# Kernel tuning notes

Hardware: AMD Instinct MI355X
Metric: run time of the kernel (lower is better)

## Reference

```python
import jax, jax.numpy as jnp
import numpy as np

K_PRE = 500        # pre-NMS candidates per class (static-shape stand-in for boolean filter)
MAX_DET = 300      # max_detections_per_images
SCORE_THR = 0.05
NMS_THR = 0.5
MIN_SIZE = 0.01    # remove_small_boxes
BBOX_CLAMP = float(np.log(1000.0 / 16.0))


def setup_inputs():
    key = jax.random.key(0)
    k1, k2, k3, k4, k5, k6 = jax.random.split(key, 6)
    B, A, C = 2, 120000, 80
    H, W = 600, 960
    deltas = jax.random.normal(k1, (B, A, 4), jnp.float32) * 0.5
    scores = jax.random.uniform(k2, (B, A, C), jnp.float32)        # post-sigmoid class scores
    # realistic anchors: centers inside the image, sizes in [16, 256]
    cx = jax.random.uniform(k3, (B, A), jnp.float32) * W
    cy = jax.random.uniform(k4, (B, A), jnp.float32) * H
    aw = 16.0 + jax.random.uniform(k5, (B, A), jnp.float32) * 240.0
    ah = 16.0 + jax.random.uniform(k6, (B, A), jnp.float32) * 240.0
    anchors = jnp.stack([cx - aw / 2, cy - ah / 2, cx + aw / 2, cy + ah / 2], axis=-1)
    return {"deltas": deltas, "scores": scores, "anchors": anchors, "img_h": H, "img_w": W}


def _decode(deltas, anchors):
    # activ_2_bbox: standard dx,dy,dw,dh decode against xyxy anchors
    aw = anchors[..., 2] - anchors[..., 0]
    ah = anchors[..., 3] - anchors[..., 1]
    acx = anchors[..., 0] + 0.5 * aw
    acy = anchors[..., 1] + 0.5 * ah
    dx, dy = deltas[..., 0], deltas[..., 1]
    dw = jnp.minimum(deltas[..., 2], BBOX_CLAMP)
    dh = jnp.minimum(deltas[..., 3], BBOX_CLAMP)
    pcx = dx * aw + acx
    pcy = dy * ah + acy
    pw = jnp.exp(dw) * aw
    ph = jnp.exp(dh) * ah
    return jnp.stack([pcx - 0.5 * pw, pcy - 0.5 * ph, pcx + 0.5 * pw, pcy + 0.5 * ph], axis=-1)


def _iou(b):  # b: [K,4] -> [K,K]
    area = (b[:, 2] - b[:, 0]) * (b[:, 3] - b[:, 1])
    lt = jnp.maximum(b[:, None, :2], b[None, :, :2])
    rb = jnp.minimum(b[:, None, 2:], b[None, :, 2:])
    wh = jnp.maximum(rb - lt, 0.0)
    inter = wh[..., 0] * wh[..., 1]
    return inter / jnp.maximum(area[:, None] + area[None, :] - inter, 1e-9)


def _per_class(boxes, valid_size, scores_c):
    # boxes [A,4], valid_size [A] bool, scores_c [A]
    valid = valid_size & (scores_c > SCORE_THR)
    masked = jnp.where(valid, scores_c, -1.0)
    top_scores, idx = jax.lax.top_k(masked, K_PRE)      # sorted desc
    cboxes = boxes[idx]                                  # [K,4]
    cvalid = top_scores > SCORE_THR
    iou = _iou(cboxes)
    rng = jnp.arange(K_PRE)

    def body(i, keep):
        sup = keep[i] & (iou[i] > NMS_THR) & (rng > i)
        return keep & ~sup

    keep = jax.lax.stop_gradient(jax.lax.fori_loop(0, K_PRE, body, cvalid))
    # move kept detections to the front preserving score order, take first MAX_DET
    order = jnp.argsort(jnp.where(keep, rng, rng + K_PRE))[:MAX_DET]
    kb = cboxes[order]
    ks = top_scores[order]
    kv = keep[order]
    return jnp.concatenate(
        [jnp.where(kv[:, None], kb, 0.0), jnp.where(kv, ks, -1.0)[:, None]], axis=-1
    )  # [MAX_DET, 5] = (x1,y1,x2,y2,score); score=-1 marks padding


def _per_image(deltas_i, scores_i, anchors_i, img_h, img_w):
    boxes = _decode(deltas_i, anchors_i)  # [A,4]
    x1 = jnp.clip(boxes[..., 0], 0.0, float(img_w))
    y1 = jnp.clip(boxes[..., 1], 0.0, float(img_h))
    x2 = jnp.clip(boxes[..., 2], 0.0, float(img_w))
    y2 = jnp.clip(boxes[..., 3], 0.0, float(img_h))
    boxes = jnp.stack([x1, y1, x2, y2], axis=-1)
    valid_size = ((x2 - x1) >= MIN_SIZE) & ((y2 - y1) >= MIN_SIZE)
    return jax.vmap(_per_class, in_axes=(None, None, 1))(boxes, valid_size, scores_i)


def reference(deltas, scores, anchors, img_h, img_w):
    f = lambda d, s, a: _per_image(d, s, a, img_h, img_w)
    return jax.vmap(f)(deltas, scores, anchors)  # [B, C, MAX_DET, 5]
```

## Files before the change

kernel.cpp:

```cpp
#include <hip/hip_runtime.h>
#include <hip/hip_bf16.h>
#include <math.h>

#define BB 2
#define AA 120000
#define CC 80
#define K_PRE 500
#define MAX_DET 300
#define CAP 2048
#define NB2 256
#define SPEC_BIN 254
#define HB 1200
#define QPB 4000
#define APB 200
#define LBUF_G 512
#define SPLIT 4
#define TRI_W 2304

#define OFF_BOXES   0
#define OFF_VALID   3840000
#define OFF_HIST    4080000
#define OFF_CNT     4161920
#define OFF_CAND    4163200
#define OFF_SUPT    0

__global__ __launch_bounds__(256) void k_fused(
    const float* __restrict__ deltas, const float* __restrict__ anchors,
    const float* __restrict__ scores,
    const int* __restrict__ ih, const int* __restrict__ iw,
    float* __restrict__ boxes, unsigned char* __restrict__ valid,
    unsigned int* __restrict__ cnt, unsigned long long* __restrict__ cand)
{
    __shared__ unsigned char lvalid[APB];
    __shared__ unsigned long long lkey[LBUF_G];
    __shared__ unsigned short lcls[LBUF_G];
    __shared__ unsigned int lcnt[CC];
    __shared__ unsigned int lbase[CC];
    __shared__ unsigned int ltot;

    int blk   = blockIdx.x;
    int b     = blk / (HB / BB);
    int abase = blk * APB;
    int start = blk * QPB;
    int end   = start + QPB;

    if (threadIdx.x < CC) lcnt[threadIdx.x] = 0u;
    if (threadIdx.x == 0) ltot = 0u;

    if (threadIdx.x < APB) {
        int a = abase + threadIdx.x;
        float4 d  = ((const float4*)deltas)[a];
        float4 an = ((const float4*)anchors)[a];

        const float CLAMPF = (float)4.135166556742356;
        double W = (double)(*iw);
        double H = (double)(*ih);

        double aw  = (double)an.z - (double)an.x;
        double ah  = (double)an.w - (double)an.y;
        double acx = (double)an.x + 0.5 * aw;
        double acy = (double)an.y + 0.5 * ah;

        double dw = fmin((double)d.z, (double)CLAMPF);
        double dh = fmin((double)d.w, (double)CLAMPF);

        double pcx = (double)d.x * aw + acx;
        double pcy = (double)d.y * ah + acy;
        double pw  = exp(dw) * aw;
        double ph  = exp(dh) * ah;

        float x1 = (float)fmin(fmax(pcx - 0.5 * pw, 0.0), W);
        float y1 = (float)fmin(fmax(pcy - 0.5 * ph, 0.0), H);
        float x2 = (float)fmin(fmax(pcx + 0.5 * pw, 0.0), W);
        float y2 = (float)fmin(fmax(pcy + 0.5 * ph, 0.0), H);

        float4 bb; bb.x = x1; bb.y = y1; bb.z = x2; bb.w = y2;
        ((float4*)boxes)[a] = bb;
        unsigned char v = (((x2 - x1) >= 0.01f) && ((y2 - y1) >= 0.01f)) ? 1 : 0;
        valid[a] = v;
        lvalid[threadIdx.x] = v;
    }
    __syncthreads();

    const float4* s4 = (const float4*)scores;
    const float THRF = (float)SPEC_BIN;

    for (int i0 = start + threadIdx.x; i0 < end; i0 += 256 * 8) {
        int   ids[8];
        bool  has[8];
        float4 s[8];
        #pragma unroll
        for (int u = 0; u < 8; ++u) {
            int id = i0 + u * 256;
            has[u] = id < end;
            ids[u] = has[u] ? id : start;
        }
        #pragma unroll
        for (int u = 0; u < 8; ++u) s[u] = s4[ids[u]];
        #pragma unroll
        for (int u = 0; u < 8; ++u) {
            if (!has[u]) continue;
            float4 sv = s[u];
            float mx = fmaxf(fmaxf(sv.x, sv.y), fmaxf(sv.z, sv.w));
            if (mx * 256.0f >= THRF) {
                int rel = ids[u] - start;
                int la  = rel / 20;
                if (lvalid[la]) {
                    int q = rel % 20;
                    unsigned int ai = (unsigned int)(abase + la - b * AA);
                    unsigned long long lokey = (unsigned long long)(~ai);
                    float cv[4] = {sv.x, sv.y, sv.z, sv.w};
                    #pragma unroll
                    for (int cl = 0; cl < 4; ++cl) {
                        float sc = cv[cl];
                        if (sc * 256.0f >= THRF) {
                            int c = 4 * q + cl;
                            unsigned long long key =
                                (((unsigned long long)__float_as_uint(sc)) << 32) | lokey;
                            unsigned int p = atomicAdd(&ltot, 1u);
                            if (p < LBUF_G) {
                                lkey[p] = key;
                                lcls[p] = (unsigned short)c;
                                atomicAdd(&lcnt[c], 1u);
                            } else {
                                unsigned int pos = atomicAdd(&cnt[b * CC + c], 1u);
                                if (pos < CAP)
                                    cand[((size_t)(b * CC + c)) * CAP + pos] = key;
                            }
                        }
                    }
                }
            }
        }
    }
    __syncthreads();

    if (threadIdx.x < CC) {
        unsigned int nn = lcnt[threadIdx.x];
        if (nn) lbase[threadIdx.x] = atomicAdd(&cnt[b * CC + threadIdx.x], nn);
    }
    __syncthreads();

    unsigned int tot = min(ltot, (unsigned int)LBUF_G);
    for (unsigned int t = threadIdx.x; t < tot; t += 256) {
        int c = lcls[t];
        unsigned int pos = atomicAdd(&lbase[c], 1u);
        if (pos < CAP)
            cand[((size_t)(b * CC + c)) * CAP + pos] = lkey[t];
    }
}

__global__ __launch_bounds__(1024) void k_sortcut(
    const float* __restrict__ boxes, const float* __restrict__ scores,
    const unsigned char* __restrict__ valid,
    const unsigned int* __restrict__ cnt, unsigned long long* __restrict__ cand)
{
    __shared__ unsigned long long kb[2][2048];
    __shared__ unsigned int lh32[NB2];
    __shared__ int best;
    __shared__ unsigned int lpos;

    int bc = blockIdx.x;
    int b  = bc / CC;
    int c  = bc % CC;
    int i  = threadIdx.x;
    unsigned long long* cp = cand + (size_t)bc * CAP;

    int n = (int)cnt[bc];
    if (n < K_PRE || n > CAP) {
        for (int t = i; t < NB2; t += 1024) lh32[t] = 0u;
        if (i == 0) { best = 0; lpos = 0u; }
        __syncthreads();
        for (int a = i; a < AA; a += 1024) {
            if (valid[b * AA + a]) {
                float sc = scores[((size_t)(b * AA + a)) * CC + c];
                if (sc > 0.05f) {
                    int bn = min((int)(sc * 256.0f), 255);
                    atomicAdd(&lh32[bn], 1u);
                }
            }
        }
        __syncthreads();
        if (i < NB2) {
            unsigned int s = 0;
            for (int j = i; j < NB2; ++j) s += lh32[j];
            if (s >= K_PRE) atomicMax(&best, i);
        }
        __syncthreads();
        int cut = best;
        for (int a = i; a < AA; a += 1024) {
            if (valid[b * AA + a]) {
                float sc = scores[((size_t)(b * AA + a)) * CC + c];
                if (sc > 0.05f) {
                    int bn = min((int)(sc * 256.0f), 255);
                    if (bn >= cut) {
                        unsigned int p = atomicAdd(&lpos, 1u);
                        if (p < CAP)
                            cp[p] = (((unsigned long long)__float_as_uint(sc)) << 32)
                                    | (unsigned long long)(~(unsigned int)a);
                    }
                }
            }
        }
        __syncthreads();
        n = (int)min(lpos, (unsigned int)CAP);
    }

    unsigned long long key;

    if (n <= 1024) {
        key = (i < n) ? cp[i] : 0ull;
        int p = 0;
        for (unsigned int k = 2; k <= 1024; k <<= 1) {
            bool up = ((i & k) == 0);
            for (unsigned int j = k >> 1; j > 0; j >>= 1) {
                unsigned long long other;
                if (j >= 64) {
                    kb[p][i] = key;
                    __syncthreads();
                    other = kb[p][i ^ j];
                    p ^= 1;
                } else {
                    other = __shfl_xor(key, (int)j);
                }
                bool lower = ((i & j) == 0);
                bool keep_max = (lower == up);
                bool mine_big = key > other;
                key = (keep_max == mine_big) ? key : other;
            }
        }
    } else {
        unsigned long long kA = (i < n) ? cp[i] : 0ull;
        unsigned long long kB = (i + 1024 < n) ? cp[i + 1024] : 0ull;
        int tA = i, tB = i + 1024;
        int p = 0;
        for (unsigned int k = 2; k <= 2048; k <<= 1) {
            for (unsigned int j = k >> 1; j > 0; j >>= 1) {
                if (j == 1024) {
                    unsigned long long mx = (kA > kB) ? kA : kB;
                    unsigned long long mn = (kA > kB) ? kB : kA;
                    kA = mx; kB = mn;
                } else if (j >= 64) {
                    kb[p][tA] = kA; kb[p][tB] = kB;
                    __syncthreads();
                    unsigned long long oA = kb[p][tA ^ (int)j];
                    unsigned long long oB = kb[p][tB ^ (int)j];
                    p ^= 1;
                    { bool up = ((tA & k) == 0), lo = ((tA & j) == 0);
                      bool km = (lo == up), mb = kA > oA; kA = (km == mb) ? kA : oA; }
                    { bool up = ((tB & k) == 0), lo = ((tB & j) == 0);
                      bool km = (lo == up), mb = kB > oB; kB = (km == mb) ? kB : oB; }
                } else {
                    unsigned long long oA = __shfl_xor(kA, (int)j);
                    unsigned long long oB = __shfl_xor(kB, (int)j);
                    { bool up = ((tA & k) == 0), lo = ((tA & j) == 0);
                      bool km = (lo == up), mb = kA > oA; kA = (km == mb) ? kA : oA; }
                    { bool up = ((tB & k) == 0), lo = ((tB & j) == 0);
                      bool km = (lo == up), mb = kB > oB; kB = (km == mb) ? kB : oB; }
                }
            }
        }
        key = kA;
    }

    float4* sbox = (float4*)cp;
    float*  ssc  = (float*)(cp + 1024);
    int*    nvp  = (int*)(cp + 1280);
    if (i < 512) {
        bool v = (key != 0ull);
        float sc = v ? __uint_as_float((unsigned int)(key >> 32)) : -1.0f;
        int a = v ? (int)(~(unsigned int)key) : 0;
        float4 bb = make_float4(0.f, 0.f, 0.f, 0.f);
        if (v && i < K_PRE) bb = ((const float4*)boxes)[(size_t)b * AA + a];
        sbox[i] = bb;
        ssc[i] = sc;
    }
    if (i == 0) nvp[0] = min(n, K_PRE);
}

__global__ __launch_bounds__(512) void k_mask(
    const unsigned long long* __restrict__ cand,
    unsigned long long* __restrict__ supTg)
{
    __shared__ float4 box4[512];
    __shared__ float  ar[512];

    int bc = blockIdx.x >> 2;
    int s  = blockIdx.x & (SPLIT - 1);
    int tid = threadIdx.x;
    const unsigned long long* cp = cand + (size_t)bc * CAP;

    float4 bl = ((const float4*)cp)[tid];
    box4[tid] = bl;
    float ia = (bl.z - bl.x) * (bl.w - bl.y);
    ar[tid] = ia;
    __syncthreads();

    int nv = ((const int*)(cp + 1280))[0];
    int wave = tid >> 6, lane = tid & 63;
    int ii = tid;
    float4 bi = bl;
    unsigned long long* sp = supTg + (size_t)bc * TRI_W;

    for (int j = wave * 64 + s; j < 512; j += SPLIT) {
        float4 bj = box4[j];
        float ja = ar[j];
        bool p = false;
        if (ii < j && j < nv) {
            float ltx = fmaxf(bi.x, bj.x);
            float lty = fmaxf(bi.y, bj.y);
            float rbx = fminf(bi.z, bj.z);
            float rby = fminf(bi.w, bj.w);
            float wx = fmaxf(rbx - ltx, 0.0f);
            float wy = fmaxf(rby - lty, 0.0f);
            float inter = wx * wy;
            float iou = inter / fmaxf(ia + ja - inter, 1e-9f);
            p = iou > 0.5f;
        }
        unsigned long long m = __ballot(p);
        if (lane == 0) {
            int g = j >> 6;
            int base = 64 * ((g * (g + 1)) >> 1) + (j & 63) * (g + 1);
            sp[base + wave] = m;
        }
    }
}

__global__ __launch_bounds__(512) void k_greedy(
    const unsigned long long* __restrict__ cand,
    const unsigned long long* __restrict__ supTg, float* __restrict__ out)
{
    __shared__ unsigned long long supT[512 * 9];
    __shared__ float4 box4[512];
    __shared__ float  scs[512];
    __shared__ unsigned long long keepsh[8];
    __shared__ int pfx[9];

    int bc = blockIdx.x;
    int tid = threadIdx.x;
    const unsigned long long* cp = cand + (size_t)bc * CAP;

    box4[tid] = ((const float4*)cp)[tid];
    scs[tid]  = ((const float*)(cp + 1024))[tid];
    int nv    = ((const int*)(cp + 1280))[0];

    const unsigned long long* sp = supTg + (size_t)bc * TRI_W;
    {
        int j = tid;
        int g = j >> 6;
        int base = 64 * ((g * (g + 1)) >> 1) + (j & 63) * (g + 1);
        for (int w = 0; w <= g; ++w) supT[j * 9 + w] = sp[base + w];
    }
    __syncthreads();

    if (tid < 64) {
        int l = tid;
        unsigned long long kept[8];
        #pragma unroll
        for (int w = 0; w < 8; ++w) {
            int j = w * 64 + l;
            bool vj = j < nv;
            bool ext = false;
            #pragma unroll
            for (int w2 = 0; w2 < 8; ++w2)
                if (w2 < w) ext = ext || ((supT[j * 9 + w2] & kept[w2]) != 0ull);
            unsigned long long intra = supT[j * 9 + w];
            bool base = vj && !ext;
            unsigned long long kw = __ballot(base);
            for (int r = 0; r < 64; ++r) {
                bool k2 = base && ((intra & kw) == 0ull);
                unsigned long long nkw = __ballot(k2);
                if (nkw == kw) break;
                kw = nkw;
            }
            kept[w] = kw;
        }
        if (l < 8) keepsh[l] = kept[l];
    }
    __syncthreads();

    if (tid == 0) {
        int s = 0;
        for (int w = 0; w < 8; ++w) { pfx[w] = s; s += __popcll(keepsh[w]); }
        pfx[8] = s;
    }
    __syncthreads();

    int total_kept = pfx[8];
    if (tid < K_PRE) {
        int t = tid;
        int w = t >> 6, bit = t & 63;
        unsigned long long kw = keepsh[w];
        bool kv = (kw >> bit) & 1ull;
        int kb2 = pfx[w] + __popcll(kw & ((bit == 0) ? 0ull : ((1ull << bit) - 1ull)));
        int p = kv ? kb2 : (total_kept + (t - kb2));
        if (p < MAX_DET) {
            float* o = out + ((size_t)bc * MAX_DET + p) * 5;
            if (kv) {
                float4 bb = box4[t];
                o[0] = bb.x; o[1] = bb.y; o[2] = bb.z; o[3] = bb.w; o[4] = scs[t];
            } else {
                o[0] = 0.f; o[1] = 0.f; o[2] = 0.f; o[3] = 0.f; o[4] = -1.0f;
            }
        }
    }
}

extern "C" void kernel_launch(void* const* d_in, const int* in_sizes, int n_in,
                              void* d_out, int out_size, void* d_ws, size_t ws_size,
                              hipStream_t stream)
{
    const float* deltas  = (const float*)d_in[0];
    const float* scores  = (const float*)d_in[1];
    const float* anchors = (const float*)d_in[2];
    const int*   ih      = (const int*)d_in[3];
    const int*   iw      = (const int*)d_in[4];
    float* out = (float*)d_out;

    char* w = (char*)d_ws;
    float*              boxes  = (float*)(w + OFF_BOXES);
    unsigned char*      valid  = (unsigned char*)(w + OFF_VALID);
    unsigned int*       cnt    = (unsigned int*)(w + OFF_CNT);
    unsigned long long* cand   = (unsigned long long*)(w + OFF_CAND);
    unsigned long long* supTg  = (unsigned long long*)(w + OFF_SUPT);

    hipMemsetAsync(cnt, 0, BB * CC * sizeof(unsigned int), stream);
    k_fused<<<HB, 256, 0, stream>>>(deltas, anchors, scores, ih, iw,
                                    boxes, valid, cnt, cand);
    k_sortcut<<<BB * CC, 1024, 0, stream>>>(boxes, scores, valid, cnt, cand);
    k_mask<<<BB * CC * SPLIT, 512, 0, stream>>>(cand, supTg);
    k_greedy<<<BB * CC, 512, 0, stream>>>(cand, supTg, out);
}
```

Before: 184.5 us.

## Fuse sort, IoU mask and greedy NMS into one per-class kernel

Merges the sort/cut, suppression-mask and greedy-selection kernels into a single 1024-thread kernel per (image, class). Sorted boxes and the triangular suppression mask now stay in shared memory instead of going through global memory. This removes two kernel launches and the global writes and reads between them. In exchange the mask step runs on only 160 blocks instead of 640 split blocks, which lowers parallelism, and the larger shared-memory footprint may reduce occupancy.

```diff
diff --git a/kernel.cpp b/kernel.cpp
--- a/kernel.cpp
+++ b/kernel.cpp
@@ -14,15 +14,11 @@
 #define QPB 4000
 #define APB 200
 #define LBUF_G 512
-#define SPLIT 4
-#define TRI_W 2304
 
 #define OFF_BOXES   0
 #define OFF_VALID   3840000
-#define OFF_HIST    4080000
 #define OFF_CNT     4161920
 #define OFF_CAND    4163200
-#define OFF_SUPT    0
 
 __global__ __launch_bounds__(256) void k_fused(
     const float* __restrict__ deltas, const float* __restrict__ anchors,
@@ -150,24 +146,32 @@
     }
 }
 
-__global__ __launch_bounds__(1024) void k_sortcut(
+__global__ __launch_bounds__(1024) void k_nms2(
     const float* __restrict__ boxes, const float* __restrict__ scores,
     const unsigned char* __restrict__ valid,
-    const unsigned int* __restrict__ cnt, unsigned long long* __restrict__ cand)
+    const unsigned int* __restrict__ cnt, const unsigned long long* __restrict__ cand,
+    float* __restrict__ out)
 {
     __shared__ unsigned long long kb[2][2048];
     __shared__ unsigned int lh32[NB2];
     __shared__ int best;
     __shared__ unsigned int lpos;
+    __shared__ float4 box4[512];
+    __shared__ float  ar[512];
+    __shared__ float  scs[512];
+    __shared__ unsigned long long supT[512 * 9];
+    __shared__ unsigned long long keepsh[8];
+    __shared__ int pfx[9];
 
     int bc = blockIdx.x;
     int b  = bc / CC;
     int c  = bc % CC;
     int i  = threadIdx.x;
-    unsigned long long* cp = cand + (size_t)bc * CAP;
+    const unsigned long long* cp = cand + (size_t)bc * CAP;
 
     int n = (int)cnt[bc];
     if (n < K_PRE || n > CAP) {
+        unsigned long long* cpw = (unsigned long long*)cp;
         for (int t = i; t < NB2; t += 1024) lh32[t] = 0u;
         if (i == 0) { best = 0; lpos = 0u; }
         __syncthreads();
@@ -196,8 +200,8 @@
                     if (bn >= cut) {
                         unsigned int p = atomicAdd(&lpos, 1u);
                         if (p < CAP)
-                            cp[p] = (((unsigned long long)__float_as_uint(sc)) << 32)
-                                    | (unsigned long long)(~(unsigned int)a);
+                            cpw[p] = (((unsigned long long)__float_as_uint(sc)) << 32)
+                                     | (unsigned long long)(~(unsigned int)a);
                     }
                 }
             }
@@ -263,98 +267,50 @@
         key = kA;
     }
 
-    float4* sbox = (float4*)cp;
-    float*  ssc  = (float*)(cp + 1024);
-    int*    nvp  = (int*)(cp + 1280);
     if (i < 512) {
         bool v = (key != 0ull);
-        float sc = v ? __uint_as_float((unsigned int)(key >> 32)) : -1.0f;
+        scs[i] = v ? __uint_as_float((unsigned int)(key >> 32)) : -1.0f;
         int a = v ? (int)(~(unsigned int)key) : 0;
         float4 bb = make_float4(0.f, 0.f, 0.f, 0.f);
         if (v && i < K_PRE) bb = ((const float4*)boxes)[(size_t)b * AA + a];
-        sbox[i] = bb;
-        ssc[i] = sc;
-    }
-    if (i == 0) nvp[0] = min(n, K_PRE);
-}
-
-__global__ __launch_bounds__(512) void k_mask(
-    const unsigned long long* __restrict__ cand,
-    unsigned long long* __restrict__ supTg)
-{
-    __shared__ float4 box4[512];
-    __shared__ float  ar[512];
-
-    int bc = blockIdx.x >> 2;
-    int s  = blockIdx.x & (SPLIT - 1);
-    int tid = threadIdx.x;
-    const unsigned long long* cp = cand + (size_t)bc * CAP;
-
-    float4 bl = ((const float4*)cp)[tid];
-    box4[tid] = bl;
-    float ia = (bl.z - bl.x) * (bl.w - bl.y);
-    ar[tid] = ia;
-    __syncthreads();
-
-    int nv = ((const int*)(cp + 1280))[0];
-    int wave = tid >> 6, lane = tid & 63;
-    int ii = tid;
-    float4 bi = bl;
-    unsigned long long* sp = supTg + (size_t)bc * TRI_W;
-
-    for (int j = wave * 64 + s; j < 512; j += SPLIT) {
-        float4 bj = box4[j];
-        float ja = ar[j];
-        bool p = false;
-        if (ii < j && j < nv) {
-            float ltx = fmaxf(bi.x, bj.x);
-            float lty = fmaxf(bi.y, bj.y);
-            float rbx = fminf(bi.z, bj.z);
-            float rby = fminf(bi.w, bj.w);
-            float wx = fmaxf(rbx - ltx, 0.0f);
-            float wy = fmaxf(rby - lty, 0.0f);
-            float inter = wx * wy;
-            float iou = inter / fmaxf(ia + ja - inter, 1e-9f);
-            p = iou > 0.5f;
-        }
-        unsigned long long m = __ballot(p);
-        if (lane == 0) {
-            int g = j >> 6;
-            int base = 64 * ((g * (g + 1)) >> 1) + (j & 63) * (g + 1);
-            sp[base + wave] = m;
-        }
-    }
-}
-
-__global__ __launch_bounds__(512) void k_greedy(
-    const unsigned long long* __restrict__ cand,
-    const unsigned long long* __restrict__ supTg, float* __restrict__ out)
-{
-    __shared__ unsigned long long supT[512 * 9];
-    __shared__ float4 box4[512];
-    __shared__ float  scs[512];
-    __shared__ unsigned long long keepsh[8];
-    __shared__ int pfx[9];
-
-    int bc = blockIdx.x;
-    int tid = threadIdx.x;
-    const unsigned long long* cp = cand + (size_t)bc * CAP;
-
-    box4[tid] = ((const float4*)cp)[tid];
-    scs[tid]  = ((const float*)(cp + 1024))[tid];
-    int nv    = ((const int*)(cp + 1280))[0];
-
-    const unsigned long long* sp = supTg + (size_t)bc * TRI_W;
+        box4[i] = bb;
+        ar[i] = (bb.z - bb.x) * (bb.w - bb.y);
+    }
+    __syncthreads();
+
+    int nv = min(n, K_PRE);
+
     {
-        int j = tid;
-        int g = j >> 6;
-        int base = 64 * ((g * (g + 1)) >> 1) + (j & 63) * (g + 1);
-        for (int w = 0; w <= g; ++w) supT[j * 9 + w] = sp[base + w];
-    }
-    __syncthreads();
-
-    if (tid < 64) {
-        int l = tid;
+        int wave = threadIdx.x >> 6;
+        int lane = threadIdx.x & 63;
+        for (int iw = 0; iw < 8; ++iw) {
+            int ii = iw * 64 + lane;
+            float4 bi = box4[ii];
+            float ia = ar[ii];
+            for (int j = iw * 64 + wave; j < 512; j += 16) {
+                float4 bj = box4[j];
+                float ja = ar[j];
+                bool p = false;
+                if (ii < j && j < nv) {
+                    float ltx = fmaxf(bi.x, bj.x);
+                    float lty = fmaxf(bi.y, bj.y);
+                    float rbx = fminf(bi.z, bj.z);
+                    float rby = fminf(bi.w, bj.w);
+                    float wx = fmaxf(rbx - ltx, 0.0f);
+                    float wy = fmaxf(rby - lty, 0.0f);
+                    float inter = wx * wy;
+                    float iou = inter / fmaxf(ia + ja - inter, 1e-9f);
+                    p = iou > 0.5f;
+                }
+                unsigned long long m = __ballot(p);
+                if (lane == 0) supT[j * 9 + iw] = m;
+            }
+        }
+    }
+    __syncthreads();
+
+    if (threadIdx.x < 64) {
+        int l = threadIdx.x;
         unsigned long long kept[8];
         #pragma unroll
         for (int w = 0; w < 8; ++w) {
@@ -379,7 +335,7 @@
     }
     __syncthreads();
 
-    if (tid == 0) {
+    if (threadIdx.x == 0) {
         int s = 0;
         for (int w = 0; w < 8; ++w) { pfx[w] = s; s += __popcll(keepsh[w]); }
         pfx[8] = s;
@@ -387,8 +343,8 @@
     __syncthreads();
 
     int total_kept = pfx[8];
-    if (tid < K_PRE) {
-        int t = tid;
+    if (threadIdx.x < K_PRE) {
+        int t = threadIdx.x;
         int w = t >> 6, bit = t & 63;
         unsigned long long kw = keepsh[w];
         bool kv = (kw >> bit) & 1ull;
@@ -422,12 +378,9 @@
     unsigned char*      valid  = (unsigned char*)(w + OFF_VALID);
     unsigned int*       cnt    = (unsigned int*)(w + OFF_CNT);
     unsigned long long* cand   = (unsigned long long*)(w + OFF_CAND);
-    unsigned long long* supTg  = (unsigned long long*)(w + OFF_SUPT);
 
     hipMemsetAsync(cnt, 0, BB * CC * sizeof(unsigned int), stream);
     k_fused<<<HB, 256, 0, stream>>>(deltas, anchors, scores, ih, iw,
                                     boxes, valid, cnt, cand);
-    k_sortcut<<<BB * CC, 1024, 0, stream>>>(boxes, scores, valid, cnt, cand);
-    k_mask<<<BB * CC * SPLIT, 512, 0, stream>>>(cand, supTg);
-    k_greedy<<<BB * CC, 512, 0, stream>>>(cand, supTg, out);
+    k_nms2<<<BB * CC, 1024, 0, stream>>>(boxes, scores, valid, cnt, cand, out);
 }
```

Result: faster. 180.5 us (-2.1%).
